# Performance work log

Measured on AMD Instinct MI355X. Metric: run time of the kernel, lower is better.

## Reference

```python
import jax, jax.numpy as jnp
import numpy as np

RADIUS = 0.3
NSAMPLE = 16
NPOINT = 256
EPS = 1e-5


def setup_inputs() -> dict:
    key = jax.random.key(0)
    ks = jax.random.split(key, 12)
    B, N, C = 16, 16384, 288
    d = {
        "xyz": jax.random.uniform(ks[0], (B, N, 3), jnp.float32),
        "features": jax.random.normal(ks[1], (B, C, N), jnp.float32),
    }
    cin = [C + 3, C, C]  # use_xyz adds 3 to first SharedMLP width
    for i in range(3):
        d[f"W{i}"] = jax.random.normal(ks[2 + i], (C, cin[i]), jnp.float32) / np.float32(np.sqrt(cin[i]))
        d[f"g{i}"] = jnp.ones((C,), jnp.float32)
        d[f"b{i}"] = jnp.zeros((C,), jnp.float32)
        d[f"m{i}"] = jax.random.normal(ks[5 + i], (C,), jnp.float32) * 0.1
        d[f"v{i}"] = jax.random.uniform(ks[8 + i], (C,), jnp.float32, minval=0.5, maxval=1.5)
    return d


def fps(xyz, npoint):
    """Farthest point sampling. xyz: (B,N,3) -> inds (B,npoint) int32."""
    B, N, _ = xyz.shape
    d0 = jnp.full((B, N), 1e10, xyz.dtype)
    i0 = jnp.zeros((B,), jnp.int32)  # CUDA kernel starts from index 0

    def step(carry, _):
        dist, idx = carry
        cur = jnp.take_along_axis(xyz, idx[:, None, None], axis=1)  # (B,1,3)
        d = jnp.sum((xyz - cur) ** 2, axis=-1)  # (B,N)
        dist = jnp.minimum(dist, d)
        nxt = jnp.argmax(dist, axis=-1).astype(jnp.int32)
        return (dist, nxt), idx

    _, inds = jax.lax.scan(step, (d0, i0), None, length=npoint)
    return inds.T  # (B, npoint)


def ball_query(xyz, new_xyz):
    """xyz: (B,N,3), new_xyz: (B,S,3) -> idx (B,S,NSAMPLE) int32.
    First NSAMPLE in-radius indices; pad with the first found index (CUDA semantics)."""
    N = xyz.shape[1]
    d2 = jnp.sum((new_xyz[:, :, None, :] - xyz[:, None, :, :]) ** 2, axis=-1)  # (B,S,N)
    mask = d2 < RADIUS * RADIUS
    cand = jnp.where(mask, jnp.arange(N, dtype=jnp.int32), jnp.int32(N))
    cand = jnp.sort(cand, axis=-1)[..., :NSAMPLE]
    first = cand[..., :1]
    return jnp.where(cand == N, first, cand)


def _mlp_bn_relu(h, W, g, b, m, v):
    # 1x1 Conv2d (no bias) + BatchNorm (running stats) + ReLU on (B,C,S,K)
    h = jnp.einsum('oc,bcsk->bosk', W, h)
    scale = (g * jax.lax.rsqrt(v + EPS))[:, None, None]
    return jax.nn.relu((h - m[:, None, None]) * scale + b[:, None, None])


def reference(xyz, features, W0, g0, b0, m0, v0, W1, g1, b1, m1, v1, W2, g2, b2, m2, v2):
    inds = fps(xyz, NPOINT)                                   # (B,S)
    new_xyz = jax.vmap(lambda p, i: p[i])(xyz, inds)          # (B,S,3)
    idx = ball_query(xyz, new_xyz)                            # (B,S,K)
    g_xyz = jax.vmap(lambda p, i: p[i])(xyz, idx)             # (B,S,K,3)
    g_xyz = (g_xyz - new_xyz[:, :, None, :]) / RADIUS         # normalize_xyz
    g_feat = jax.vmap(lambda f, i: f[:, i])(features, idx)    # (B,C,S,K)
    h = jnp.concatenate([jnp.transpose(g_xyz, (0, 3, 1, 2)), g_feat], axis=1)  # (B,C+3,S,K)
    for (W, g, b, m, v) in ((W0, g0, b0, m0, v0), (W1, g1, b1, m1, v1), (W2, g2, b2, m2, v2)):
        h = _mlp_bn_relu(h, W, g, b, m, v)
    new_features = jnp.max(h, axis=-1)                        # (B,C,S) max-pool over nsample
    return new_xyz, new_features, inds
```

## Files before the change

### kernel.cpp

```cpp
#include <hip/hip_runtime.h>
#include <hip/hip_bf16.h>
#include <string.h>

#define NPT   16384
#define NBAT  16
#define CH    288
#define SP    256
#define KS    16
#define OFF_FEAT 12288L
#define OFF_IND  1191936L

__device__ __forceinline__ float bfbits(unsigned short u){
  unsigned int x = ((unsigned int)u) << 16; float f; __builtin_memcpy(&f,&x,4); return f;
}
__device__ __forceinline__ float ldf(const void* p, long i, int isb){
  if (isb) return __bfloat162float(((const __hip_bfloat16*)p)[i]);
  return ((const float*)p)[i];
}
__device__ __forceinline__ void sto(void* p, long i, float v, int isb){
  if (isb) ((__hip_bfloat16*)p)[i] = __float2bfloat16(v);
  else     ((float*)p)[i] = v;
}
__device__ __forceinline__ void gload_lds(const void* g, void* l){
  __builtin_amdgcn_global_load_lds((const __attribute__((address_space(1))) void*)g,
      (__attribute__((address_space(3))) void*)l, 16, 0, 0);
}
__device__ __forceinline__ unsigned spread4(unsigned x){
  return (x&1u) | ((x&2u)<<2) | ((x&4u)<<4) | ((x&8u)<<6);
}

typedef __attribute__((ext_vector_type(8))) short bf16x8;
typedef __attribute__((ext_vector_type(4))) float f32x4;

__global__ void detect_k(const void* __restrict__ xyz, int* __restrict__ flag){
  __shared__ float red[256];
  const int t = threadIdx.x;
  const unsigned short* u = (const unsigned short*)xyz;
  float m = 0.f;
  for (int i = t; i < 4096; i += 256){
    float f = fabsf(bfbits(u[i]));
    if (f != f) f = 1e30f;
    m = fmaxf(m, f);
  }
  red[t] = m; __syncthreads();
  for (int s = 128; s; s >>= 1){ if (t < s) red[t] = fmaxf(red[t], red[t+s]); __syncthreads(); }
  if (t == 0) *flag = (red[0] < 2.0f) ? 1 : 0;
}

__global__ __launch_bounds__(256) void cvtxyz_k(const void* __restrict__ xyz,
    const int* __restrict__ flag, float* __restrict__ X, float* __restrict__ Y,
    float* __restrict__ Z){
  const int e = blockIdx.x*256 + threadIdx.x;
  const int isb = *flag;
  float v = ldf(xyz, e, isb);
  int b = e / (NPT*3), r = e - b*(NPT*3), i = r/3, c = r - i*3;
  float* P = (c==0) ? X : ((c==1) ? Y : Z);
  P[b*NPT + i] = v;
}

__global__ __launch_bounds__(256) void cvtw_k(const void* __restrict__ W,
    const void* __restrict__ g, const void* __restrict__ bb,
    const void* __restrict__ m, const void* __restrict__ v,
    const int* __restrict__ flag, __hip_bfloat16* __restrict__ Wbf,
    float* __restrict__ scale, float* __restrict__ shift, int Kin){
  const int isb = *flag;
  const int idx = blockIdx.x*256 + threadIdx.x;
  if (idx < 288*296){
    int o = idx / 296, k = idx - o*296;
    float val = (k < Kin) ? ldf(W, (long)o*Kin + k, isb) : 0.f;
    Wbf[idx] = __float2bfloat16(val);
  }
  if (idx < 288){
    float sc = ldf(g, idx, isb) * rsqrtf(ldf(v, idx, isb) + 1e-5f);
    scale[idx] = sc;
    shift[idx] = ldf(bb, idx, isb) - ldf(m, idx, isb)*sc;
  }
}

__global__ __launch_bounds__(1024) void sort_k(const float* __restrict__ X,
    const float* __restrict__ Y, const float* __restrict__ Z,
    float* __restrict__ X2, float* __restrict__ Y2, float* __restrict__ Z2,
    int* __restrict__ I2){
  __shared__ int hist[4096];
  __shared__ int wtot[16];
  const int b = blockIdx.x, t = threadIdx.x, base = b*NPT;
  for (int j = t; j < 4096; j += 1024) hist[j] = 0;
  __syncthreads();
  int cell[16]; float lx[16], ly[16], lz[16];
  #pragma unroll
  for (int i=0;i<16;i++){
    const int id = t + i*1024;
    float x = X[base+id], y = Y[base+id], z = Z[base+id];
    lx[i]=x; ly[i]=y; lz[i]=z;
    int cx = (int)(x*16.f); cx = cx<0?0:(cx>15?15:cx);
    int cy = (int)(y*16.f); cy = cy<0?0:(cy>15?15:cy);
    int cz = (int)(z*16.f); cz = cz<0?0:(cz>15?15:cz);
    cell[i] = (int)(spread4((unsigned)cx) | (spread4((unsigned)cy)<<1) | (spread4((unsigned)cz)<<2));
    atomicAdd(&hist[cell[i]], 1);
  }
  __syncthreads();
  int s0 = hist[t*4], s1 = hist[t*4+1], s2 = hist[t*4+2], s3 = hist[t*4+3];
  int ls = s0+s1+s2+s3;
  int sc = ls;
  #pragma unroll
  for (int off=1; off<64; off<<=1){
    int o = __shfl_up(sc, off, 64);
    if ((t&63) >= off) sc += o;
  }
  if ((t&63) == 63) wtot[t>>6] = sc;
  __syncthreads();
  int wpre = 0;
  #pragma unroll
  for (int w=0; w<16; w++) wpre += (w < (t>>6)) ? wtot[w] : 0;
  const int ebase = wpre + sc - ls;
  hist[t*4]   = ebase;
  hist[t*4+1] = ebase + s0;
  hist[t*4+2] = ebase + s0 + s1;
  hist[t*4+3] = ebase + s0 + s1 + s2;
  __syncthreads();
  #pragma unroll
  for (int i=0;i<16;i++){
    const int dst = atomicAdd(&hist[cell[i]], 1);
    X2[base+dst] = lx[i]; Y2[base+dst] = ly[i]; Z2[base+dst] = lz[i];
    I2[base+dst] = t + i*1024;
  }
}

__global__ __launch_bounds__(1024) __attribute__((amdgpu_waves_per_eu(4,4)))
void fps_k(const float* __restrict__ X, const float* __restrict__ Y,
    const float* __restrict__ Z,
    const float* __restrict__ X2, const float* __restrict__ Y2,
    const float* __restrict__ Z2, const int* __restrict__ I2,
    const int* __restrict__ flag, float* __restrict__ nxyz, void* __restrict__ dout){
  #pragma clang fp contract(off)
  const int b = blockIdx.x, t = threadIdx.x;
  const int base = b*NPT;
  const int lane = t & 63, wid = t >> 6;
  float px[16], py[16], pz[16], dist[16];
  unsigned int li[16];
  const int p0 = base + wid*1024 + lane;
  #pragma unroll
  for (int i=0;i<16;i++){
    px[i] = X2[p0 + i*64];
    py[i] = Y2[p0 + i*64];
    pz[i] = Z2[p0 + i*64];
    li[i] = 16383u - (unsigned)I2[p0 + i*64];
    dist[i] = 1e10f;
  }
  float bxn=px[0],bxx=px[0],byn=py[0],byx=py[0],bzn=pz[0],bzx=pz[0];
  #pragma unroll
  for (int i=1;i<16;i++){
    bxn=fminf(bxn,px[i]); bxx=fmaxf(bxx,px[i]);
    byn=fminf(byn,py[i]); byx=fmaxf(byx,py[i]);
    bzn=fminf(bzn,pz[i]); bzx=fmaxf(bzx,pz[i]);
  }
  #pragma unroll
  for (int off=32; off; off>>=1){
    bxn=fminf(bxn,__shfl_xor(bxn,off,64)); bxx=fmaxf(bxx,__shfl_xor(bxx,off,64));
    byn=fminf(byn,__shfl_xor(byn,off,64)); byx=fmaxf(byx,__shfl_xor(byx,off,64));
    bzn=fminf(bzn,__shfl_xor(bzn,off,64)); bzx=fmaxf(bzx,__shfl_xor(bzx,off,64));
  }
  __shared__ unsigned long long slot[2][16];
  __shared__ float ox[SP], oy[SP], oz[SP];
  __shared__ int   oi[SP];
  float cx = X[base], cy = Y[base], cz = Z[base];
  int cur = 0;
  unsigned long long wkey = 0ull;
  float wavemax = 1e30f;
  for (int it=0; it<SP; it++){
    if (t == 0){ ox[it]=cx; oy[it]=cy; oz[it]=cz; oi[it]=cur; }
    float ddx = fmaxf(fmaxf(bxn-cx, cx-bxx), 0.f);
    float ddy = fmaxf(fmaxf(byn-cy, cy-byx), 0.f);
    float ddz = fmaxf(fmaxf(bzn-cz, cz-bzx), 0.f);
    float lb = ddx*ddx + ddy*ddy + ddz*ddz;
    if (!(lb * 0.9999f > wavemax)){
      unsigned long long best = 0ull;
      #pragma unroll
      for (int i=0;i<16;i++){
        float dx = px[i]-cx, dy = py[i]-cy, dz = pz[i]-cz;
        float d2 = dx*dx + dy*dy; d2 = d2 + dz*dz;
        float dn = fminf(dist[i], d2); dist[i] = dn;
        unsigned long long key = ((unsigned long long)__float_as_uint(dn) << 32)
                               | (unsigned long long)li[i];
        best = (key > best) ? key : best;
      }
      #pragma unroll
      for (int off=32; off; off>>=1){
        unsigned long long o = __shfl_xor(best, off, 64);
        best = (o > best) ? o : best;
      }
      wkey = best;
      wavemax = __uint_as_float((unsigned)(best >> 32));
    }
    const int p = it & 1;
    if (lane == 0) slot[p][wid] = wkey;
    __syncthreads();
    unsigned long long g = slot[p][lane & 15];
    #pragma unroll
    for (int m=8; m; m>>=1){
      unsigned long long o = __shfl_xor(g, m, 64);
      g = (o > g) ? o : g;
    }
    cur = 16383 - (int)(unsigned)g;
    cur = __builtin_amdgcn_readfirstlane(cur);
    cx = X[base+cur]; cy = Y[base+cur]; cz = Z[base+cur];
  }
  __syncthreads();
  if (t < SP){
    const int isb = *flag;
    const long bs = (long)b*SP + t;
    float fx=ox[t], fy=oy[t], fz=oz[t]; int ii=oi[t];
    nxyz[bs*3+0]=fx; nxyz[bs*3+1]=fy; nxyz[bs*3+2]=fz;
    sto(dout, bs*3+0, fx, isb);
    sto(dout, bs*3+1, fy, isb);
    sto(dout, bs*3+2, fz, isb);
    sto(dout, OFF_IND + bs, (float)ii, isb);
  }
}

__global__ __launch_bounds__(256) void ballq_k(const float* __restrict__ X,
    const float* __restrict__ Y, const float* __restrict__ Z,
    const float* __restrict__ nxyz, int* __restrict__ bidx){
  #pragma clang fp contract(off)
  const int gw = (blockIdx.x*256 + threadIdx.x) >> 6;
  const int lane = threadIdx.x & 63;
  const int b = gw >> 8, base = b*NPT;
  const float cx = nxyz[gw*3+0], cy = nxyz[gw*3+1], cz = nxyz[gw*3+2];
  int cnt = 0, first = 0; bool havef = false;
  for (int st = 0; st < NPT && cnt < KS; st += 64){
    const int id = st + lane;
    float dx = X[base+id]-cx, dy = Y[base+id]-cy, dz = Z[base+id]-cz;
    float d2 = dx*dx + dy*dy; d2 = d2 + dz*dz;
    unsigned long long mk = __ballot(d2 <= 0.09f);
    if (mk){
      if (!havef){ first = st + __builtin_ctzll(mk); havef = true; }
      int rank = cnt + __popcll(mk & ((1ull<<lane)-1ull));
      if (((mk>>lane)&1ull) && rank < KS) bidx[gw*KS + rank] = id;
      cnt += __popcll(mk);
    }
  }
  if (cnt < KS && lane >= cnt && lane < KS) bidx[gw*KS + lane] = first;
}

__global__ __launch_bounds__(256) void gather_k(const void* __restrict__ xyz,
    const void* __restrict__ feat, const int* __restrict__ flag,
    const int* __restrict__ bidx, const float* __restrict__ nxyz,
    __hip_bfloat16* __restrict__ h0){
  __shared__ __hip_bfloat16 tile[64*296];
  const int isb = *flag;
  const int t = threadIdx.x, n0 = blockIdx.x*64;
  const int nl = t >> 2, cg = t & 3;
  const int n = n0 + nl, b = n >> 12, s = n >> 4;
  const int id = bidx[n];
  for (int j=0; j<74; j++){
    int c = cg*74 + j;
    float vv = 0.f;
    if (c < 3)       vv = (ldf(xyz, ((long)b*NPT + id)*3 + c, isb) - nxyz[(long)s*3 + c]) / 0.3f;
    else if (c < 291) vv = ldf(feat, ((long)b*CH + (c-3))*(long)NPT + id, isb);
    tile[nl*296 + c] = __float2bfloat16(vv);
  }
  __syncthreads();
  const uint4* src = (const uint4*)tile;
  uint4* dst = (uint4*)((char*)h0 + (long)n0*592);
  for (int j = t; j < 2368; j += 256) dst[j] = src[j];
}

__global__ __launch_bounds__(256, 2) void gemm_k(
    const __hip_bfloat16* __restrict__ A, int astr,
    const __hip_bfloat16* __restrict__ W,
    const float* __restrict__ scale, const float* __restrict__ shift,
    __hip_bfloat16* __restrict__ Out, int ostr,
    int ktiles, int kvalid){
  extern __shared__ char lds[];
  const int t = threadIdx.x, lane = t & 63, wid = t >> 6;
  const int wm = wid & 1, wo = wid >> 1;
  const int bx = blockIdx.x, by = blockIdx.y;
  {
    const char* src = (const char*)(A + (long)bx*128*astr);
    const int chunks = (128*astr*2) >> 10;
    for (int c = wid; c < chunks; c += 4)
      gload_lds(src + c*1024 + lane*16, lds + c*1024);
  }
  f32x4 acc[4][3];
  #pragma unroll
  for (int mf=0; mf<4; mf++)
    #pragma unroll
    for (int of=0; of<3; of++) acc[mf][of] = (f32x4){0.f,0.f,0.f,0.f};

  const int mrow  = wm*64 + (lane & 15);
  const int kg    = (lane >> 4) * 8;
  const int obase = by*96 + wo*48 + (lane & 15);
  __syncthreads();

  for (int kt = 0; kt < ktiles; kt++){
    const int k0 = kt*32 + kg;
    const bool z = (k0 >= kvalid);
    const int k0c = z ? 0 : k0;
    bf16x8 a[4], bf[3];
    #pragma unroll
    for (int mf=0; mf<4; mf++)
      a[mf] = *(const bf16x8*)(lds + ((long)(mrow + mf*16)*astr + k0c)*2);
    if (z){
      bf16x8 zz = {0,0,0,0,0,0,0,0};
      #pragma unroll
      for (int mf=0; mf<4; mf++) a[mf] = zz;
    }
    #pragma unroll
    for (int of=0; of<3; of++)
      bf[of] = *(const bf16x8*)(W + (long)(obase + of*16)*296 + k0c);
    #pragma unroll
    for (int mf=0; mf<4; mf++)
      #pragma unroll
      for (int of=0; of<3; of++)
        acc[mf][of] = __builtin_amdgcn_mfma_f32_16x16x32_bf16(a[mf], bf[of], acc[mf][of], 0, 0, 0);
  }

  float sc[3], sh[3];
  #pragma unroll
  for (int of=0; of<3; of++){ sc[of] = scale[obase + of*16]; sh[of] = shift[obase + of*16]; }
  #pragma unroll
  for (int mf=0; mf<4; mf++)
    #pragma unroll
    for (int of=0; of<3; of++)
      #pragma unroll
      for (int r=0; r<4; r++){
        const long row = (long)bx*128 + wm*64 + mf*16 + (lane>>4)*4 + r;
        const int o = obase + of*16;
        float vv = acc[mf][of][r]*sc[of] + sh[of];
        Out[row*ostr + o] = __float2bfloat16(fmaxf(vv, 0.f));
      }
}

__global__ __launch_bounds__(256) void maxk_k(const __hip_bfloat16* __restrict__ h,
    const int* __restrict__ flag, void* __restrict__ dout){
  __shared__ __hip_bfloat16 tile[128*288];
  const int isb = *flag;
  const int t = threadIdx.x;
  const int b = blockIdx.x >> 5, s0 = (blockIdx.x & 31)*8;
  const long n0 = (long)b*4096 + (long)s0*16;
  {
    const char* src = (const char*)(h + n0*288);
    for (int c = (t>>6); c < 72; c += 4)
      gload_lds(src + c*1024 + (t&63)*16, (char*)tile + c*1024);
  }
  __syncthreads();
  for (int o = t; o < 288; o += 256){
    float mx[8];
    #pragma unroll
    for (int sl=0; sl<8; sl++){
      float m = -1e30f;
      #pragma unroll
      for (int kk=0; kk<16; kk++)
        m = fmaxf(m, __bfloat162float(tile[(sl*16 + kk)*288 + o]));
      mx[sl] = m;
    }
    const long e0 = OFF_FEAT + (long)b*73728 + (long)o*256 + s0;
    if (isb){
      unsigned short u[8];
      #pragma unroll
      for (int sl=0; sl<8; sl++){
        __hip_bfloat16 hb = __float2bfloat16(mx[sl]);
        __builtin_memcpy(&u[sl], &hb, 2);
      }
      uint4 pk; __builtin_memcpy(&pk, u, 16);
      *(uint4*)((__hip_bfloat16*)dout + e0) = pk;
    } else {
      float* fo = (float*)dout + e0;
      *(float4*)fo     = make_float4(mx[0],mx[1],mx[2],mx[3]);
      *(float4*)(fo+4) = make_float4(mx[4],mx[5],mx[6],mx[7]);
    }
  }
}

extern "C" void kernel_launch(void* const* d_in, const int* in_sizes, int n_in,
                              void* d_out, int out_size, void* d_ws, size_t ws_size,
                              hipStream_t stream){
  const void* xyz  = d_in[0];
  const void* feat = d_in[1];
  const void* W0 = d_in[2];  const void* g0 = d_in[3];  const void* b0 = d_in[4];
  const void* m0 = d_in[5];  const void* v0 = d_in[6];
  const void* W1 = d_in[7];  const void* g1 = d_in[8];  const void* b1 = d_in[9];
  const void* m1 = d_in[10]; const void* v1 = d_in[11];
  const void* W2 = d_in[12]; const void* g2 = d_in[13]; const void* b2 = d_in[14];
  const void* m2 = d_in[15]; const void* v2 = d_in[16];

  char* ws = (char*)d_ws;
  int*   flag  = (int*)ws;
  float* sc0   = (float*)(ws + 64);
  float* sh0   = sc0 + 288;
  float* sc1   = sc0 + 576;  float* sh1 = sc0 + 864;
  float* sc2   = sc0 + 1152; float* sh2 = sc0 + 1440;
  __hip_bfloat16* Wb0 = (__hip_bfloat16*)(ws + 7040);
  __hip_bfloat16* Wb1 = Wb0 + 288*296;
  __hip_bfloat16* Wb2 = Wb1 + 288*296;
  float* nxyz = (float*)(ws + 518656);
  int*   bidx = (int*)(ws + 567808);
  float* X    = (float*)(ws + 1048576);
  float* Y    = X + NBAT*NPT;
  float* Z    = Y + NBAT*NPT;
  __hip_bfloat16* bufA = (__hip_bfloat16*)(ws + 1048576);
  __hip_bfloat16* bufB = (__hip_bfloat16*)(ws + 1048576 + 38797312);
  float* X2 = (float*)bufB;
  float* Y2 = X2 + NBAT*NPT;
  float* Z2 = Y2 + NBAT*NPT;
  int*   I2 = (int*)(Z2 + NBAT*NPT);

  detect_k<<<1, 256, 0, stream>>>(xyz, flag);
  cvtxyz_k<<<3072, 256, 0, stream>>>(xyz, flag, X, Y, Z);
  cvtw_k<<<333, 256, 0, stream>>>(W0, g0, b0, m0, v0, flag, Wb0, sc0, sh0, 291);
  cvtw_k<<<333, 256, 0, stream>>>(W1, g1, b1, m1, v1, flag, Wb1, sc1, sh1, 288);
  cvtw_k<<<333, 256, 0, stream>>>(W2, g2, b2, m2, v2, flag, Wb2, sc2, sh2, 288);
  sort_k<<<NBAT, 1024, 0, stream>>>(X, Y, Z, X2, Y2, Z2, I2);
  fps_k<<<NBAT, 1024, 0, stream>>>(X, Y, Z, X2, Y2, Z2, I2, flag, nxyz, d_out);
  ballq_k<<<1024, 256, 0, stream>>>(X, Y, Z, nxyz, bidx);
  gather_k<<<1024, 256, 0, stream>>>(xyz, feat, flag, bidx, nxyz, bufA);
  gemm_k<<<dim3(512,3), 256, 128*296*2, stream>>>(bufA, 296, Wb0, sc0, sh0, bufB, 288, 10, 296);
  gemm_k<<<dim3(512,3), 256, 128*288*2, stream>>>(bufB, 288, Wb1, sc1, sh1, bufA, 296, 9, 288);
  gemm_k<<<dim3(512,3), 256, 128*296*2, stream>>>(bufA, 296, Wb2, sc2, sh2, bufB, 288, 9, 288);
  maxk_k<<<512, 256, 0, stream>>>(bufB, flag, d_out);
}
```

Measured before the change: 1.012 ms.

## Pack FPS point math into float2 vectors and fetch centroid as float4

The FPS inner loop now holds points as float2 pairs so the compiler can emit packed FP32 subtract, multiply and add, roughly halving the per-iteration VALU instruction count on the serial critical path. A packed xyz float4 array is also built in the conversion kernel so each iteration's centroid lookup is one 16-byte load instead of three dependent scalar loads. The conversion kernel now handles one point per thread, and the new array sits in workspace after X, Y, Z. Packed math could change register allocation under the fixed waves-per-EU setting.

```diff
diff --git a/kernel.cpp b/kernel.cpp
--- a/kernel.cpp
+++ b/kernel.cpp
@@ -31,6 +31,7 @@
 
 typedef __attribute__((ext_vector_type(8))) short bf16x8;
 typedef __attribute__((ext_vector_type(4))) float f32x4;
+typedef __attribute__((ext_vector_type(2))) float f32x2;
 
 __global__ void detect_k(const void* __restrict__ xyz, int* __restrict__ flag){
   __shared__ float red[256];
@@ -49,13 +50,14 @@
 
 __global__ __launch_bounds__(256) void cvtxyz_k(const void* __restrict__ xyz,
     const int* __restrict__ flag, float* __restrict__ X, float* __restrict__ Y,
-    float* __restrict__ Z){
-  const int e = blockIdx.x*256 + threadIdx.x;
+    float* __restrict__ Z, float4* __restrict__ P4){
+  const int n = blockIdx.x*256 + threadIdx.x;
   const int isb = *flag;
-  float v = ldf(xyz, e, isb);
-  int b = e / (NPT*3), r = e - b*(NPT*3), i = r/3, c = r - i*3;
-  float* P = (c==0) ? X : ((c==1) ? Y : Z);
-  P[b*NPT + i] = v;
+  float x = ldf(xyz, (long)n*3+0, isb);
+  float y = ldf(xyz, (long)n*3+1, isb);
+  float z = ldf(xyz, (long)n*3+2, isb);
+  X[n] = x; Y[n] = y; Z[n] = z;
+  P4[n] = make_float4(x, y, z, 0.f);
 }
 
 __global__ __launch_bounds__(256) void cvtw_k(const void* __restrict__ W,
@@ -127,8 +129,7 @@
 }
 
 __global__ __launch_bounds__(1024) __attribute__((amdgpu_waves_per_eu(4,4)))
-void fps_k(const float* __restrict__ X, const float* __restrict__ Y,
-    const float* __restrict__ Z,
+void fps_k(const float4* __restrict__ P4,
     const float* __restrict__ X2, const float* __restrict__ Y2,
     const float* __restrict__ Z2, const int* __restrict__ I2,
     const int* __restrict__ flag, float* __restrict__ nxyz, void* __restrict__ dout){
@@ -136,23 +137,24 @@
   const int b = blockIdx.x, t = threadIdx.x;
   const int base = b*NPT;
   const int lane = t & 63, wid = t >> 6;
-  float px[16], py[16], pz[16], dist[16];
-  unsigned int li[16];
+  f32x2 px[8], py[8], pz[8], ds[8];
+  unsigned li[16];
   const int p0 = base + wid*1024 + lane;
   #pragma unroll
-  for (int i=0;i<16;i++){
-    px[i] = X2[p0 + i*64];
-    py[i] = Y2[p0 + i*64];
-    pz[i] = Z2[p0 + i*64];
-    li[i] = 16383u - (unsigned)I2[p0 + i*64];
-    dist[i] = 1e10f;
-  }
-  float bxn=px[0],bxx=px[0],byn=py[0],byx=py[0],bzn=pz[0],bzx=pz[0];
-  #pragma unroll
-  for (int i=1;i<16;i++){
-    bxn=fminf(bxn,px[i]); bxx=fmaxf(bxx,px[i]);
-    byn=fminf(byn,py[i]); byx=fmaxf(byx,py[i]);
-    bzn=fminf(bzn,pz[i]); bzx=fmaxf(bzx,pz[i]);
+  for (int j=0;j<8;j++){
+    px[j] = (f32x2){X2[p0 + (2*j)*64], X2[p0 + (2*j+1)*64]};
+    py[j] = (f32x2){Y2[p0 + (2*j)*64], Y2[p0 + (2*j+1)*64]};
+    pz[j] = (f32x2){Z2[p0 + (2*j)*64], Z2[p0 + (2*j+1)*64]};
+    li[2*j]   = 16383u - (unsigned)I2[p0 + (2*j)*64];
+    li[2*j+1] = 16383u - (unsigned)I2[p0 + (2*j+1)*64];
+    ds[j] = (f32x2){1e10f, 1e10f};
+  }
+  float bxn=px[0].x,bxx=px[0].x,byn=py[0].x,byx=py[0].x,bzn=pz[0].x,bzx=pz[0].x;
+  #pragma unroll
+  for (int j=0;j<8;j++){
+    bxn=fminf(bxn,fminf(px[j].x,px[j].y)); bxx=fmaxf(bxx,fmaxf(px[j].x,px[j].y));
+    byn=fminf(byn,fminf(py[j].x,py[j].y)); byx=fmaxf(byx,fmaxf(py[j].x,py[j].y));
+    bzn=fminf(bzn,fminf(pz[j].x,pz[j].y)); bzx=fmaxf(bzx,fmaxf(pz[j].x,pz[j].y));
   }
   #pragma unroll
   for (int off=32; off; off>>=1){
@@ -163,7 +165,8 @@
   __shared__ unsigned long long slot[2][16];
   __shared__ float ox[SP], oy[SP], oz[SP];
   __shared__ int   oi[SP];
-  float cx = X[base], cy = Y[base], cz = Z[base];
+  float4 c4 = P4[base];
+  float cx = c4.x, cy = c4.y, cz = c4.z;
   int cur = 0;
   unsigned long long wkey = 0ull;
   float wavemax = 1e30f;
@@ -174,15 +177,21 @@
     float ddz = fmaxf(fmaxf(bzn-cz, cz-bzx), 0.f);
     float lb = ddx*ddx + ddy*ddy + ddz*ddz;
     if (!(lb * 0.9999f > wavemax)){
+      const f32x2 Cx = {cx,cx}, Cy = {cy,cy}, Cz = {cz,cz};
       unsigned long long best = 0ull;
       #pragma unroll
-      for (int i=0;i<16;i++){
-        float dx = px[i]-cx, dy = py[i]-cy, dz = pz[i]-cz;
-        float d2 = dx*dx + dy*dy; d2 = d2 + dz*dz;
-        float dn = fminf(dist[i], d2); dist[i] = dn;
-        unsigned long long key = ((unsigned long long)__float_as_uint(dn) << 32)
-                               | (unsigned long long)li[i];
-        best = (key > best) ? key : best;
+      for (int j=0;j<8;j++){
+        f32x2 dx = px[j]-Cx, dy = py[j]-Cy, dz = pz[j]-Cz;
+        f32x2 m0 = dx*dx, m1 = dy*dy, m2 = dz*dz;
+        f32x2 d2 = (m0+m1)+m2;
+        f32x2 dn = __builtin_elementwise_min(ds[j], d2);
+        ds[j] = dn;
+        unsigned long long k0 = ((unsigned long long)__float_as_uint(dn.x)<<32)
+                              | (unsigned long long)li[2*j];
+        unsigned long long k1 = ((unsigned long long)__float_as_uint(dn.y)<<32)
+                              | (unsigned long long)li[2*j+1];
+        best = (k0 > best) ? k0 : best;
+        best = (k1 > best) ? k1 : best;
       }
       #pragma unroll
       for (int off=32; off; off>>=1){
@@ -203,7 +212,8 @@
     }
     cur = 16383 - (int)(unsigned)g;
     cur = __builtin_amdgcn_readfirstlane(cur);
-    cx = X[base+cur]; cy = Y[base+cur]; cz = Z[base+cur];
+    c4 = P4[base+cur];
+    cx = c4.x; cy = c4.y; cz = c4.z;
   }
   __syncthreads();
   if (t < SP){
@@ -398,6 +408,7 @@
   float* X    = (float*)(ws + 1048576);
   float* Y    = X + NBAT*NPT;
   float* Z    = Y + NBAT*NPT;
+  float4* P4  = (float4*)(ws + 1048576 + 3145728);
   __hip_bfloat16* bufA = (__hip_bfloat16*)(ws + 1048576);
   __hip_bfloat16* bufB = (__hip_bfloat16*)(ws + 1048576 + 38797312);
   float* X2 = (float*)bufB;
@@ -406,12 +417,12 @@
   int*   I2 = (int*)(Z2 + NBAT*NPT);
 
   detect_k<<<1, 256, 0, stream>>>(xyz, flag);
-  cvtxyz_k<<<3072, 256, 0, stream>>>(xyz, flag, X, Y, Z);
+  cvtxyz_k<<<1024, 256, 0, stream>>>(xyz, flag, X, Y, Z, P4);
   cvtw_k<<<333, 256, 0, stream>>>(W0, g0, b0, m0, v0, flag, Wb0, sc0, sh0, 291);
   cvtw_k<<<333, 256, 0, stream>>>(W1, g1, b1, m1, v1, flag, Wb1, sc1, sh1, 288);
   cvtw_k<<<333, 256, 0, stream>>>(W2, g2, b2, m2, v2, flag, Wb2, sc2, sh2, 288);
   sort_k<<<NBAT, 1024, 0, stream>>>(X, Y, Z, X2, Y2, Z2, I2);
-  fps_k<<<NBAT, 1024, 0, stream>>>(X, Y, Z, X2, Y2, Z2, I2, flag, nxyz, d_out);
+  fps_k<<<NBAT, 1024, 0, stream>>>(P4, X2, Y2, Z2, I2, flag, nxyz, d_out);
   ballq_k<<<1024, 256, 0, stream>>>(X, Y, Z, nxyz, bidx);
   gather_k<<<1024, 256, 0, stream>>>(xyz, feat, flag, bidx, nxyz, bufA);
   gemm_k<<<dim3(512,3), 256, 128*296*2, stream>>>(bufA, 296, Wb0, sc0, sh0, bufB, 288, 10, 296);
```

After: 1.009 ms. About the same (-0.3%).
